# Kernel optimization log

Hardware: AMD Instinct MI355X
Metric: run time of the kernel (lower is better)

## Reference

```python
import jax, jax.numpy as jnp
import numpy as np
import math

B, N, D, H, FFN = 4, 2048, 512, 8, 2048
DK = D // H
EPS = 1e-5


def _layer_norm(x, g, b):
    mu = jnp.mean(x, axis=-1, keepdims=True)
    var = jnp.mean((x - mu) ** 2, axis=-1, keepdims=True)
    return (x - mu) * jax.lax.rsqrt(var + EPS) * g + b


def _rotate_half(x):
    h = x.shape[-1] // 2
    return jnp.concatenate([-x[..., h:], x[..., :h]], axis=-1)


def _rope(q, k, positions):
    # q, k: (B, H, N, DK); positions: (B, N) int
    inv_freq = 1.0 / (10000.0 ** (jnp.arange(0, DK, 2, dtype=jnp.float32) / DK))  # (DK/2,)
    ang = positions[:, None, :, None].astype(jnp.float32) * inv_freq  # (B,1,N,DK/2)
    cos = jnp.concatenate([jnp.cos(ang), jnp.cos(ang)], axis=-1)  # (B,1,N,DK)
    sin = jnp.concatenate([jnp.sin(ang), jnp.sin(ang)], axis=-1)
    q = q * cos + _rotate_half(q) * sin
    k = k * cos + _rotate_half(k) * sin
    return q, k


def setup_inputs() -> dict:
    key = jax.random.key(0)
    ks = jax.random.split(key, 16)
    s = 0.02
    x = jax.random.normal(ks[0], (B, N, D), dtype=jnp.float32)
    # backward-looking hop mask within jobs: random boolean with True diagonal
    m = jax.random.uniform(ks[1], (B, N, N)) < 0.1
    o2o_mask = m | jnp.eye(N, dtype=bool)[None]
    positions = jax.random.randint(ks[2], (B, N), 0, N)
    params = {
        'wq': jax.random.normal(ks[3], (D, D)) * s, 'bq': jnp.zeros((D,)),
        'wk': jax.random.normal(ks[4], (D, D)) * s, 'bk': jnp.zeros((D,)),
        'wv': jax.random.normal(ks[5], (D, D)) * s, 'bv': jnp.zeros((D,)),
        'wo': jax.random.normal(ks[6], (D, D)) * s, 'bo': jnp.zeros((D,)),
        'ln1_g': jnp.ones((D,)), 'ln1_b': jnp.zeros((D,)),
        'ln2_g': jnp.ones((D,)), 'ln2_b': jnp.zeros((D,)),
        'w1': jax.random.normal(ks[7], (D, FFN)) * s, 'b1': jnp.zeros((FFN,)),
        'w2': jax.random.normal(ks[8], (FFN, D)) * s, 'b2': jnp.zeros((D,)),
    }
    return {'x': x, 'o2o_mask': o2o_mask, 'positions': positions, **params}


def reference(x, o2o_mask, positions, wq, bq, wk, bk, wv, bv, wo, bo,
              ln1_g, ln1_b, ln2_g, ln2_b, w1, b1, w2, b2):
    residual = x
    xn = _layer_norm(x, ln1_g, ln1_b)
    q = (xn @ wq + bq).reshape(B, N, H, DK).transpose(0, 2, 1, 3)
    k = (xn @ wk + bk).reshape(B, N, H, DK).transpose(0, 2, 1, 3)
    v = (xn @ wv + bv).reshape(B, N, H, DK).transpose(0, 2, 1, 3)
    q, k = _rope(q, k, positions)
    scores = jnp.einsum('bhqd,bhkd->bhqk', q, k) / math.sqrt(DK)
    scores = jnp.where(o2o_mask[:, None], scores, -jnp.inf)
    attn = jax.nn.softmax(scores, axis=-1)
    attn = jnp.where(jnp.isnan(attn), 0.0, attn)  # fully-masked rows -> 0
    attn_out = jnp.einsum('bhqk,bhkd->bhqd', attn, v)
    attn_out = attn_out.transpose(0, 2, 1, 3).reshape(B, N, D)
    x = residual + (attn_out @ wo + bo)
    residual = x
    h = _layer_norm(x, ln2_g, ln2_b)
    h = jax.nn.relu(h @ w1 + b1) @ w2 + b2
    return residual + h
```

## Files before the change

kernel.cpp:

```cpp
#include <hip/hip_runtime.h>
#include <hip/hip_bf16.h>
#include <math.h>

typedef __attribute__((ext_vector_type(8))) __bf16 bf16x8;
typedef __attribute__((ext_vector_type(4))) __bf16 bf16x4;
typedef __attribute__((ext_vector_type(4))) float f32x4;

#define B_ 4
#define N_ 2048
#define D_ 512
#define H_ 8
#define DK_ 64
#define F_ 2048

__device__ __forceinline__ void async16(const __bf16* g, __bf16* l) {
  __builtin_amdgcn_global_load_lds((const __attribute__((address_space(1))) void*)g,
                                   (__attribute__((address_space(3))) void*)l, 16, 0, 0);
}

__global__ __launch_bounds__(256) void prep_all(const float* __restrict__ wq,
                                                const float* __restrict__ wk,
                                                const float* __restrict__ wv,
                                                const float* __restrict__ wo,
                                                const float* __restrict__ w1,
                                                const float* __restrict__ w2,
                                                const float* __restrict__ bq,
                                                const float* __restrict__ bk,
                                                const float* __restrict__ bv,
                                                __bf16* __restrict__ wqkvt,
                                                __bf16* __restrict__ wot,
                                                __bf16* __restrict__ w1t,
                                                __bf16* __restrict__ w2t,
                                                float* __restrict__ bqkv) {
  const int id = blockIdx.x;
  if (id >= 768) {
    int i = (id - 768) * 256 + threadIdx.x;
    bqkv[i] = (i < 512) ? bq[i] : (i < 1024) ? bk[i - 512] : bv[i - 1024];
    return;
  }
  __shared__ float t[64][65];
  const float* in;
  __bf16* outp;
  int k0, n0, K, Nc;
  if (id < 256) {
    const float* src[4] = {wq, wk, wv, wo};
    __bf16* dst[4] = {wqkvt, wqkvt + 512 * 512, wqkvt + 1024 * 512, wot};
    int w = id >> 6, tl = id & 63;
    in = src[w]; outp = dst[w]; k0 = (tl & 7) * 64; n0 = (tl >> 3) * 64; K = 512; Nc = 512;
  } else if (id < 512) {
    int tl = id - 256;
    in = w1; outp = w1t; k0 = (tl & 7) * 64; n0 = (tl >> 3) * 64; K = 512; Nc = 2048;
  } else {
    int tl = id - 512;
    in = w2; outp = w2t; k0 = (tl & 31) * 64; n0 = (tl >> 5) * 64; K = 2048; Nc = 512;
  }
  const int c = threadIdx.x & 63, r4 = threadIdx.x >> 6;
#pragma unroll
  for (int p = 0; p < 16; p++) {
    int rr = p * 4 + r4;
    t[rr][c] = in[(size_t)(k0 + rr) * Nc + n0 + c];
  }
  __syncthreads();
#pragma unroll
  for (int p = 0; p < 16; p++) {
    int rr = p * 4 + r4;
    outp[(size_t)(n0 + rr) * K + k0 + c] = (__bf16)t[c][rr];
  }
}

__global__ __launch_bounds__(256) void build_bitmask(const int* __restrict__ mask,
                                                     unsigned long long* __restrict__ bm) {
  size_t t = (size_t)blockIdx.x * 256 + threadIdx.x;
  int m = mask[t];
  unsigned long long w = __ballot(m != 0);
  if ((threadIdx.x & 63) == 0) bm[t >> 6] = w;
}

__global__ __launch_bounds__(256) void ln_fwd(const float* __restrict__ x,
                                              const float* __restrict__ g,
                                              const float* __restrict__ b,
                                              __bf16* __restrict__ out) {
  int row = blockIdx.x * 4 + (threadIdx.x >> 6);
  int lane = threadIdx.x & 63;
  const float* xr = x + (size_t)row * D_ + lane * 8;
  float4 a0 = *(const float4*)xr;
  float4 a1 = *(const float4*)(xr + 4);
  float v[8] = {a0.x, a0.y, a0.z, a0.w, a1.x, a1.y, a1.z, a1.w};
  float s = 0.f;
#pragma unroll
  for (int i = 0; i < 8; i++) s += v[i];
#pragma unroll
  for (int off = 1; off < 64; off <<= 1) s += __shfl_xor(s, off);
  float mu = s * (1.f / D_);
  float q = 0.f;
#pragma unroll
  for (int i = 0; i < 8; i++) { float d = v[i] - mu; q += d * d; }
#pragma unroll
  for (int off = 1; off < 64; off <<= 1) q += __shfl_xor(q, off);
  float rs = rsqrtf(q * (1.f / D_) + 1e-5f);
  const float* gp = g + lane * 8;
  const float* bp = b + lane * 8;
  alignas(16) __bf16 o[8];
#pragma unroll
  for (int i = 0; i < 8; i++) o[i] = (__bf16)((v[i] - mu) * rs * gp[i] + bp[i]);
  *(bf16x8*)(out + (size_t)row * D_ + lane * 8) = *(bf16x8*)o;
}

__global__ __launch_bounds__(256) void rope_vtrans(const __bf16* __restrict__ qkv,
                                                   const int* __restrict__ pos,
                                                   __bf16* __restrict__ qo,
                                                   __bf16* __restrict__ ko,
                                                   __bf16* __restrict__ vt) {
  __shared__ __bf16 tl[64][65];
  const int id = blockIdx.x;
  if (id < 8192) {
    int t = id * 256 + threadIdx.x;
    int d = t & 31;
    int h = (t >> 5) & 7;
    int n = (t >> 8) & (N_ - 1);
    int b = t >> 19;
    const __bf16* base = qkv + (size_t)(b * N_ + n) * 1536 + h * 64 + d;
    float q1 = (float)base[0], q2 = (float)base[32];
    float k1 = (float)base[512], k2 = (float)base[544];
    float p = (float)pos[b * N_ + n];
    float inv = __expf(-(float)d * (9.210340371976184f / 32.f));
    float ang = p * inv;
    float sn, cs;
    sincosf(ang, &sn, &cs);
    const float SC = 0.18033688011112042f;
    size_t ob = ((size_t)(b * H_ + h) * N_ + n) * DK_ + d;
    qo[ob]      = (__bf16)((q1 * cs - q2 * sn) * SC);
    qo[ob + 32] = (__bf16)((q2 * cs + q1 * sn) * SC);
    ko[ob]      = (__bf16)(k1 * cs - k2 * sn);
    ko[ob + 32] = (__bf16)(k2 * cs + k1 * sn);
  } else {
    const int lin = id - 8192;
    const int n0 = (lin & 31) * 64, h = (lin >> 5) & 7, b = lin >> 8;
    const int c = threadIdx.x & 63, rr = threadIdx.x >> 6;
#pragma unroll
    for (int p = 0; p < 16; p++) {
      int i = p * 4 + rr;
      tl[i][c] = qkv[(size_t)(b * N_ + n0 + i) * 1536 + 1024 + h * 64 + c];
    }
    __syncthreads();
    size_t ob = (size_t)(b * H_ + h) * DK_ * N_;
#pragma unroll
    for (int p = 0; p < 16; p++) {
      int dd = p * 4 + rr;
      vt[ob + (size_t)dd * N_ + n0 + c] = tl[c][dd];
    }
  }
}

template <int RELU, int OBF, int RES>
__global__ __launch_bounds__(256) void gemm_bt(const __bf16* __restrict__ A,
                                               const __bf16* __restrict__ Bt,
                                               const float* __restrict__ bias,
                                               const float* __restrict__ res,
                                               void* __restrict__ Cout,
                                               int M, int N, int K) {
  __shared__ __bf16 As[2][128 * 32];
  __shared__ __bf16 Bs[2][128 * 32];
  const int tid = threadIdx.x;
  const int lane = tid & 63;
  const int wave = tid >> 6;
  const int quad = lane >> 4;
  const int l16 = lane & 15;
  const int m0 = blockIdx.y * 128;
  const int n0 = blockIdx.x * 128;
  const int wm = (wave >> 1) * 64;
  const int wn = (wave & 1) * 64;
  f32x4 acc[4][4] = {};

  const int c0 = tid, c1 = tid + 256;
  const int ar0 = c0 >> 2, ak0 = (c0 & 3) * 8;
  const int ar1 = c1 >> 2, ak1 = (c1 & 3) * 8;

  auto stage = [&](int k0, int buf) {
    async16(A + (size_t)(m0 + ar0) * K + k0 + ak0, As[buf] + c0 * 8);
    async16(A + (size_t)(m0 + ar1) * K + k0 + ak1, As[buf] + c1 * 8);
    async16(Bt + (size_t)(n0 + ar0) * K + k0 + ak0, Bs[buf] + c0 * 8);
    async16(Bt + (size_t)(n0 + ar1) * K + k0 + ak1, Bs[buf] + c1 * 8);
  };

  stage(0, 0);
  __syncthreads();
  const int niter = K >> 5;
  for (int it = 0; it < niter; it++) {
    const int buf = it & 1;
    if (it + 1 < niter) stage((it + 1) * 32, buf ^ 1);
    bf16x8 af[4], bf[4];
#pragma unroll
    for (int mi = 0; mi < 4; mi++)
      af[mi] = *(const bf16x8*)(As[buf] + (wm + mi * 16 + l16) * 32 + quad * 8);
#pragma unroll
    for (int ni = 0; ni < 4; ni++)
      bf[ni] = *(const bf16x8*)(Bs[buf] + (wn + ni * 16 + l16) * 32 + quad * 8);
#pragma unroll
    for (int mi = 0; mi < 4; mi++)
#pragma unroll
      for (int ni = 0; ni < 4; ni++)
        acc[mi][ni] = __builtin_amdgcn_mfma_f32_16x16x32_bf16(af[mi], bf[ni], acc[mi][ni], 0, 0, 0);
    __syncthreads();
  }
#pragma unroll
  for (int ni = 0; ni < 4; ni++) {
    const int col = n0 + wn + ni * 16 + l16;
    const float bv = bias[col];
#pragma unroll
    for (int mi = 0; mi < 4; mi++) {
#pragma unroll
      for (int r = 0; r < 4; r++) {
        const int row = m0 + wm + mi * 16 + quad * 4 + r;
        float v = acc[mi][ni][r] + bv;
        if (RES) v += res[(size_t)row * N + col];
        if (RELU) v = fmaxf(v, 0.f);
        if (OBF) ((__bf16*)Cout)[(size_t)row * N + col] = (__bf16)v;
        else     ((float*)Cout)[(size_t)row * N + col] = v;
      }
    }
  }
}

template <int RELU, int OBF, int RES>
__global__ __launch_bounds__(256) void gemm_bt64(const __bf16* __restrict__ A,
                                                 const __bf16* __restrict__ Bt,
                                                 const float* __restrict__ bias,
                                                 const float* __restrict__ res,
                                                 void* __restrict__ Cout,
                                                 int M, int N, int K) {
  __shared__ __bf16 As[2][128 * 32];
  __shared__ __bf16 Bs[2][64 * 32];
  const int tid = threadIdx.x;
  const int lane = tid & 63;
  const int wave = tid >> 6;
  const int quad = lane >> 4;
  const int l16 = lane & 15;
  const int m0 = blockIdx.y * 128;
  const int n0 = blockIdx.x * 64;
  const int wm = wave * 32;
  f32x4 acc[2][4] = {};

  const int ar0 = tid >> 2, ak0 = (tid & 3) * 8;

  auto stage = [&](int k0, int buf) {
    async16(A + (size_t)(m0 + ar0) * K + k0 + ak0, As[buf] + tid * 8);
    async16(A + (size_t)(m0 + 64 + ar0) * K + k0 + ak0, As[buf] + (tid + 256) * 8);
    async16(Bt + (size_t)(n0 + ar0) * K + k0 + ak0, Bs[buf] + tid * 8);
  };

  stage(0, 0);
  __syncthreads();
  const int niter = K >> 5;
  for (int it = 0; it < niter; it++) {
    const int buf = it & 1;
    if (it + 1 < niter) stage((it + 1) * 32, buf ^ 1);
    bf16x8 af[2], bf[4];
#pragma unroll
    for (int mi = 0; mi < 2; mi++)
      af[mi] = *(const bf16x8*)(As[buf] + (wm + mi * 16 + l16) * 32 + quad * 8);
#pragma unroll
    for (int ni = 0; ni < 4; ni++)
      bf[ni] = *(const bf16x8*)(Bs[buf] + (ni * 16 + l16) * 32 + quad * 8);
#pragma unroll
    for (int mi = 0; mi < 2; mi++)
#pragma unroll
      for (int ni = 0; ni < 4; ni++)
        acc[mi][ni] = __builtin_amdgcn_mfma_f32_16x16x32_bf16(af[mi], bf[ni], acc[mi][ni], 0, 0, 0);
    __syncthreads();
  }
#pragma unroll
  for (int ni = 0; ni < 4; ni++) {
    const int col = n0 + ni * 16 + l16;
    const float bv = bias[col];
#pragma unroll
    for (int mi = 0; mi < 2; mi++) {
#pragma unroll
      for (int r = 0; r < 4; r++) {
        const int row = m0 + wm + mi * 16 + quad * 4 + r;
        float v = acc[mi][ni][r] + bv;
        if (RES) v += res[(size_t)row * N + col];
        if (RELU) v = fmaxf(v, 0.f);
        if (OBF) ((__bf16*)Cout)[(size_t)row * N + col] = (__bf16)v;
        else     ((float*)Cout)[(size_t)row * N + col] = v;
      }
    }
  }
}

__global__ __launch_bounds__(512, 4) void flash_attn(const __bf16* __restrict__ q,
                                                     const __bf16* __restrict__ k,
                                                     const __bf16* __restrict__ vt,
                                                     const unsigned long long* __restrict__ bm,
                                                     __bf16* __restrict__ out) {
  const int bid = blockIdx.x;
  const int gl = ((bid & 7) << 6) | (bid >> 3);
  const int qt = gl & 15;
  const int h = (gl >> 4) & 7;
  const int b = gl >> 7;
  const int tid = threadIdx.x;
  const int lane = tid & 63, wave = tid >> 6;
  const int quad = lane >> 4, l16 = lane & 15;
  __shared__ __bf16 Ks[2][64 * 64];
  __shared__ __bf16 Vs[2][64 * 64];
  __shared__ __bf16 P[8][16 * 68];
  const size_t bh = (size_t)b * H_ + h;
  const __bf16* qp = q + (bh * N_ + qt * 128 + wave * 16) * DK_;
  bf16x8 qf[2];
#pragma unroll
  for (int ks = 0; ks < 2; ks++)
    qf[ks] = *(const bf16x8*)(qp + l16 * DK_ + ks * 32 + quad * 8);
  const __bf16* kbase = k + bh * N_ * DK_;
  const __bf16* vbase = vt + bh * DK_ * N_;
  const int qrow0 = qt * 128 + wave * 16 + l16;
  const unsigned long long* bmr = bm + (size_t)(b * N_ + qrow0) * (N_ / 64);
  const int xo = l16 & 7;

  f32x4 oacc[4] = {};
  float lsum = 0.f;

  auto stage = [&](int kt, int buf) {
    const __bf16* kg = kbase + (size_t)kt * 64 * DK_;
    const __bf16* vg = vbase + kt * 64;
    const int s = tid;
    const int r = s >> 3;
    const int j = (s & 7) ^ (r & 7);
    async16(kg + r * DK_ + j * 8, Ks[buf] + s * 8);
    async16(vg + (size_t)r * N_ + j * 8, Vs[buf] + s * 8);
  };

  stage(0, 0);
  __syncthreads();

  for (int kt = 0; kt < N_ / 64; kt++) {
    const int buf = kt & 1;
    if (kt + 1 < N_ / 64) stage(kt + 1, buf ^ 1);
    unsigned long long mw_nxt = 0;
    if (kt + 1 < N_ / 64) mw_nxt = bmr[kt + 1];

    const unsigned long long mw = bmr[kt];
    const unsigned long long mws = mw >> (quad * 4);
#pragma unroll
    for (int ci = 0; ci < 4; ci++) {
      const int row = ci * 16 + l16;
      bf16x8 kf0 = *(const bf16x8*)(Ks[buf] + (row * 8 + (quad ^ xo)) * 8);
      bf16x8 kf1 = *(const bf16x8*)(Ks[buf] + (row * 8 + ((4 + quad) ^ xo)) * 8);
      f32x4 a = {0.f, 0.f, 0.f, 0.f};
      a = __builtin_amdgcn_mfma_f32_16x16x32_bf16(kf0, qf[0], a, 0, 0, 0);
      a = __builtin_amdgcn_mfma_f32_16x16x32_bf16(kf1, qf[1], a, 0, 0, 0);
      const unsigned int nib = (unsigned int)(mws >> (ci * 16)) & 15u;
      bf16x4 pk;
#pragma unroll
      for (int r4 = 0; r4 < 4; r4++) {
        float in = ((nib >> r4) & 1u) ? a[r4] : -1e30f;
        float p = exp2f(in);
        lsum += p;
        pk[r4] = (__bf16)p;
      }
      *(bf16x4*)(&P[wave][0] + l16 * 68 + ci * 16 + quad * 4) = pk;
    }
    bf16x8 pf0 = *(const bf16x8*)(&P[wave][0] + l16 * 68 + quad * 8);
    bf16x8 pf1 = *(const bf16x8*)(&P[wave][0] + l16 * 68 + 32 + quad * 8);
#pragma unroll
    for (int ni = 0; ni < 4; ni++) {
      const int row = ni * 16 + l16;
      bf16x8 vf0 = *(const bf16x8*)(Vs[buf] + (row * 8 + (quad ^ xo)) * 8);
      bf16x8 vf1 = *(const bf16x8*)(Vs[buf] + (row * 8 + ((4 + quad) ^ xo)) * 8);
      oacc[ni] = __builtin_amdgcn_mfma_f32_16x16x32_bf16(vf0, pf0, oacc[ni], 0, 0, 0);
      oacc[ni] = __builtin_amdgcn_mfma_f32_16x16x32_bf16(vf1, pf1, oacc[ni], 0, 0, 0);
    }
    __syncthreads();
  }
  lsum += __shfl_xor(lsum, 16);
  lsum += __shfl_xor(lsum, 32);
  const float inv_l = (lsum > 0.f) ? 1.f / lsum : 0.f;
#pragma unroll
  for (int ni = 0; ni < 4; ni++) {
    bf16x4 ov;
#pragma unroll
    for (int r = 0; r < 4; r++) ov[r] = (__bf16)(oacc[ni][r] * inv_l);
    *(bf16x4*)(out + ((size_t)b * N_ + qrow0) * D_ + h * DK_ + ni * 16 + quad * 4) = ov;
  }
}

static constexpr size_t OFF_XN  = 0;
static constexpr size_t OFF_WT  = 8388608;
static constexpr size_t OFF_WO  = OFF_WT + 1572864;
static constexpr size_t OFF_W1  = OFF_WO + 524288;
static constexpr size_t OFF_W2  = OFF_W1 + 2097152;
static constexpr size_t OFF_BQ  = OFF_W2 + 2097152;
static constexpr size_t OFF_QKV = OFF_BQ + 6144;
static constexpr size_t OFF_QR  = OFF_QKV + 25165824;
static constexpr size_t OFF_KR  = OFF_QR + 8388608;
static constexpr size_t OFF_VT  = OFF_KR + 8388608;
static constexpr size_t OFF_AO  = OFF_VT + 8388608;
static constexpr size_t OFF_Y   = OFF_AO + 8388608;

extern "C" void kernel_launch(void* const* d_in, const int* in_sizes, int n_in,
                              void* d_out, int out_size, void* d_ws, size_t ws_size,
                              hipStream_t stream) {
  const float* x    = (const float*)d_in[0];
  const int*   mask = (const int*)d_in[1];
  const int*   pos  = (const int*)d_in[2];
  const float* wq   = (const float*)d_in[3];
  const float* bq   = (const float*)d_in[4];
  const float* wk   = (const float*)d_in[5];
  const float* bk   = (const float*)d_in[6];
  const float* wv   = (const float*)d_in[7];
  const float* bv   = (const float*)d_in[8];
  const float* wo   = (const float*)d_in[9];
  const float* bo   = (const float*)d_in[10];
  const float* ln1g = (const float*)d_in[11];
  const float* ln1b = (const float*)d_in[12];
  const float* ln2g = (const float*)d_in[13];
  const float* ln2b = (const float*)d_in[14];
  const float* w1   = (const float*)d_in[15];
  const float* b1   = (const float*)d_in[16];
  const float* w2   = (const float*)d_in[17];
  const float* b2   = (const float*)d_in[18];
  float* out = (float*)d_out;
  char* ws = (char*)d_ws;

  __bf16* xn    = (__bf16*)(ws + OFF_XN);
  __bf16* wqkvt = (__bf16*)(ws + OFF_WT);
  __bf16* wot   = (__bf16*)(ws + OFF_WO);
  __bf16* w1t   = (__bf16*)(ws + OFF_W1);
  __bf16* w2t   = (__bf16*)(ws + OFF_W2);
  float*  bqkv  = (float*)(ws + OFF_BQ);
  __bf16* qkv   = (__bf16*)(ws + OFF_QKV);
  __bf16* qr    = (__bf16*)(ws + OFF_QR);
  __bf16* kr    = (__bf16*)(ws + OFF_KR);
  __bf16* vt    = (__bf16*)(ws + OFF_VT);
  __bf16* attn  = (__bf16*)(ws + OFF_AO);
  float*  y     = (float*)(ws + OFF_Y);
  unsigned long long* bm = (unsigned long long*)(ws + OFF_Y);
  __bf16* hn    = xn;
  __bf16* h2    = qkv;

  dim3 b256(256);
  dim3 b512(512);
  prep_all<<<774, b256, 0, stream>>>(wq, wk, wv, wo, w1, w2, bq, bk, bv,
                                     wqkvt, wot, w1t, w2t, bqkv);
  build_bitmask<<<65536, b256, 0, stream>>>(mask, bm);
  ln_fwd<<<2048, b256, 0, stream>>>(x, ln1g, ln1b, xn);
  gemm_bt<0, 1, 0><<<dim3(12, 64), b256, 0, stream>>>(xn, wqkvt, bqkv, nullptr, qkv, 8192, 1536, 512);
  rope_vtrans<<<9216, b256, 0, stream>>>(qkv, pos, qr, kr, vt);
  flash_attn<<<512, b512, 0, stream>>>(qr, kr, vt, bm, attn);
  gemm_bt64<0, 0, 1><<<dim3(8, 64), b256, 0, stream>>>(attn, wot, bo, x, y, 8192, 512, 512);
  ln_fwd<<<2048, b256, 0, stream>>>(y, ln2g, ln2b, hn);
  gemm_bt<1, 1, 0><<<dim3(16, 64), b256, 0, stream>>>(hn, w1t, b1, nullptr, h2, 8192, 2048, 512);
  gemm_bt64<0, 0, 1><<<dim3(8, 64), b256, 0, stream>>>(h2, w2t, b2, y, out, 8192, 512, 2048);
}
```

Baseline: 379.6 us.

## Triple-buffer K/V tiles in flash attention with explicit vmcnt waits

Flash attention moves from double to triple buffering of the K and V LDS tiles. It prefetches two tiles ahead and replaces __syncthreads with a partial s_waitcnt vmcnt(3) plus s_barrier, so later loads stay in flight across the barrier. The mask word for the next tile is now loaded one iteration early. The Q prescale changes from log2(e)/8 to 1/8 and exp2f becomes __expf, which is mathematically equivalent. The cost is more LDS per block, which may limit occupancy, and redundant loads of the last tile at the end of the loop.

```diff
diff --git a/kernel.cpp b/kernel.cpp
--- a/kernel.cpp
+++ b/kernel.cpp
@@ -127,7 +127,7 @@
     float ang = p * inv;
     float sn, cs;
     sincosf(ang, &sn, &cs);
-    const float SC = 0.18033688011112042f;
+    const float SC = 0.125f;
     size_t ob = ((size_t)(b * H_ + h) * N_ + n) * DK_ + d;
     qo[ob]      = (__bf16)((q1 * cs - q2 * sn) * SC);
     qo[ob + 32] = (__bf16)((q2 * cs + q1 * sn) * SC);
@@ -301,8 +301,8 @@
   const int tid = threadIdx.x;
   const int lane = tid & 63, wave = tid >> 6;
   const int quad = lane >> 4, l16 = lane & 15;
-  __shared__ __bf16 Ks[2][64 * 64];
-  __shared__ __bf16 Vs[2][64 * 64];
+  __shared__ __bf16 Ks[3][64 * 64];
+  __shared__ __bf16 Vs[3][64 * 64];
   __shared__ __bf16 P[8][16 * 68];
   const size_t bh = (size_t)b * H_ + h;
   const __bf16* qp = q + (bh * N_ + qt * 128 + wave * 16) * DK_;
@@ -319,26 +319,30 @@
   f32x4 oacc[4] = {};
   float lsum = 0.f;
 
+  const int sr = tid >> 3;
+  const int sj = (tid & 7) ^ (sr & 7);
+  const __bf16* ksrc = kbase + sr * DK_ + sj * 8;
+  const __bf16* vsrc = vbase + (size_t)sr * N_ + sj * 8;
+
   auto stage = [&](int kt, int buf) {
-    const __bf16* kg = kbase + (size_t)kt * 64 * DK_;
-    const __bf16* vg = vbase + kt * 64;
-    const int s = tid;
-    const int r = s >> 3;
-    const int j = (s & 7) ^ (r & 7);
-    async16(kg + r * DK_ + j * 8, Ks[buf] + s * 8);
-    async16(vg + (size_t)r * N_ + j * 8, Vs[buf] + s * 8);
+    async16(ksrc + (size_t)kt * 64 * DK_, Ks[buf] + tid * 8);
+    async16(vsrc + kt * 64, Vs[buf] + tid * 8);
   };
 
   stage(0, 0);
-  __syncthreads();
-
-  for (int kt = 0; kt < N_ / 64; kt++) {
-    const int buf = kt & 1;
-    if (kt + 1 < N_ / 64) stage(kt + 1, buf ^ 1);
-    unsigned long long mw_nxt = 0;
-    if (kt + 1 < N_ / 64) mw_nxt = bmr[kt + 1];
-
-    const unsigned long long mw = bmr[kt];
+  stage(1, 1);
+  unsigned long long mw = bmr[0];
+  asm volatile("s_waitcnt vmcnt(3)" ::: "memory");
+  __builtin_amdgcn_s_barrier();
+  __builtin_amdgcn_sched_barrier(0);
+
+  for (int kt = 0; kt < 32; kt++) {
+    const int buf = kt % 3;
+    const int nstage = (kt + 2 < 32) ? kt + 2 : 31;
+    stage(nstage, (kt + 2) % 3);
+    const int nmask = (kt + 1 < 32) ? kt + 1 : 31;
+    const unsigned long long mw_nxt = bmr[nmask];
+
     const unsigned long long mws = mw >> (quad * 4);
 #pragma unroll
     for (int ci = 0; ci < 4; ci++) {
@@ -353,7 +357,7 @@
 #pragma unroll
       for (int r4 = 0; r4 < 4; r4++) {
         float in = ((nib >> r4) & 1u) ? a[r4] : -1e30f;
-        float p = exp2f(in);
+        float p = __expf(in);
         lsum += p;
         pk[r4] = (__bf16)p;
       }
@@ -369,7 +373,10 @@
       oacc[ni] = __builtin_amdgcn_mfma_f32_16x16x32_bf16(vf0, pf0, oacc[ni], 0, 0, 0);
       oacc[ni] = __builtin_amdgcn_mfma_f32_16x16x32_bf16(vf1, pf1, oacc[ni], 0, 0, 0);
     }
-    __syncthreads();
+    asm volatile("s_waitcnt vmcnt(3)" ::: "memory");
+    __builtin_amdgcn_s_barrier();
+    __builtin_amdgcn_sched_barrier(0);
+    mw = mw_nxt;
   }
   lsum += __shfl_xor(lsum, 16);
   lsum += __shfl_xor(lsum, 32);
```

Result: faster. 362.8 us (-4.4%).
